# Optimization experiments

Measured on AMD Instinct MI355X. Metric: run time of the kernel, lower is better.

Reference implementation:

```python
import jax, jax.numpy as jnp
import numpy as np

SMOOTH = 1e-5  # MONAI DiceLoss smooth_nr / smooth_dr defaults
BETA = 1.0


def setup_inputs() -> dict:
    key = jax.random.key(0)
    k1, k2, k3 = jax.random.split(key, 3)
    B, C, H, W = 8, 16, 512, 512
    outputs = jax.random.normal(k1, (B, C, H, W), dtype=jnp.float32)
    targets = jax.random.randint(k2, (B, 1, H, W), 0, C, dtype=jnp.int64)
    matrix_penalty = jax.random.uniform(k3, (C, C), dtype=jnp.float32)
    return {
        "outputs": outputs,
        "targets": targets,
        "matrix_penalty": matrix_penalty,
        "N_classes": C,
        "Npixels": H * W,
        "length_targets": B,
        "total_batch": B,
    }


def _domino_loss(outputs, matrix_penalty, t, N_classes, total_batch):
    # outputs: [B, C, H, W] logits; t: [B, H, W] int labels
    logp = jax.nn.log_softmax(outputs, axis=1)          # [B, C, H, W]
    probs = jnp.exp(logp)
    probs_bhwc = jnp.moveaxis(probs, 1, -1)             # [B, H, W, C]
    onehot = jax.nn.one_hot(t, N_classes, dtype=outputs.dtype)  # [B, H, W, C]

    # Cross-entropy term (mean over all pixels), as in CrossEntropyLoss
    ce = -jnp.mean(jnp.sum(onehot * jnp.moveaxis(logp, 1, -1), axis=-1))

    # Dice term (softmax probs vs one-hot target, per batch x class, mean)
    inter = jnp.sum(probs_bhwc * onehot, axis=(1, 2))   # [B, C]
    denom = jnp.sum(probs_bhwc, axis=(1, 2)) + jnp.sum(onehot, axis=(1, 2))
    dice = jnp.mean(1.0 - (2.0 * inter + SMOOTH) / (denom + SMOOTH))

    # DOMINO penalty: per pixel, one_hot(target)^T @ matrix_penalty @ softmax(logits)
    # = matrix_penalty[target] . probs  (gather row instead of tiny matmul)
    pen_rows = matrix_penalty[t]                        # [B, H, W, C]
    penalty = jnp.sum(pen_rows * probs_bhwc)

    return ce + dice + BETA * penalty / total_batch


def reference(outputs, targets, matrix_penalty, N_classes, Npixels, length_targets, total_batch):
    t = targets[:, 0].astype(jnp.int32)                 # [B, H, W]
    return _domino_loss(outputs, matrix_penalty, t, N_classes, total_batch)
```

## Files before the change

### kernel.cpp

```cpp
#include <hip/hip_runtime.h>

#define NC      16
#define HW      (512 * 512)
#define NB      8
#define BPB     128
#define NBLK    (NB * BPB)
#define THREADS 256
#define CHUNK   (HW / BPB)
#define VITERS  (CHUNK / (THREADS * 2))
#define SMOOTH  1e-5f

__global__ __launch_bounds__(THREADS) void domino_main(
    const float* __restrict__ logits,
    const int*   __restrict__ tgt,
    const float* __restrict__ penalty,
    float*       __restrict__ P)
{
    __shared__ float pen_t[NC * NC];
    __shared__ float red[4][34];

    const int tid = threadIdx.x;
    const int b   = blockIdx.x / BPB;
    const int blk = blockIdx.x % BPB;

    if (tid < NC * NC) {
        const int r = tid / NC, c = tid % NC;
        pen_t[c * NC + r] = penalty[tid];
    }
    __syncthreads();

    float inter_acc[NC], denom_acc[NC];
#pragma unroll
    for (int c = 0; c < NC; ++c) { inter_acc[c] = 0.f; denom_acc[c] = 0.f; }
    float ce_acc = 0.f, pen_acc = 0.f;

    const float* ob = logits + (size_t)b * NC * HW;
    const int*   tb = tgt    + (size_t)b * HW;

#pragma unroll
    for (int k = 0; k < VITERS; ++k) {
        const int g   = blk * (CHUNK / 2) + k * THREADS + tid;
        const int pix = g * 2;

        float2 x[NC];
#pragma unroll
        for (int c = 0; c < NC; ++c)
            x[c] = *(const float2*)(ob + (size_t)c * HW + pix);
        const int2 t2 = *(const int2*)(tb + pix);

#define PROC(F, TT) do {                                                    \
        const int t = (TT);                                                 \
        float m = -3.402823466e+38f;                                        \
        _Pragma("unroll")                                                   \
        for (int c = 0; c < NC; ++c) m = fmaxf(m, x[c].F);                  \
        float s = 0.f, xt = 0.f;                                            \
        _Pragma("unroll")                                                   \
        for (int c = 0; c < NC; ++c) {                                      \
            s  += __expf(x[c].F - m);                                       \
            xt += (t == c) ? x[c].F : 0.f;                                  \
        }                                                                   \
        const float inv = 1.0f / s;                                         \
        ce_acc += (__logf(s) + m) - xt;                                     \
        float pdot = 0.f;                                                   \
        _Pragma("unroll")                                                   \
        for (int c = 0; c < NC; ++c) {                                      \
            const float p = __expf(x[c].F - m) * inv;                       \
            denom_acc[c] += p + ((t == c) ? 1.f : 0.f);                     \
            inter_acc[c] += (t == c) ? p : 0.f;                             \
            pdot += pen_t[c * NC + t] * p;                                  \
        }                                                                   \
        pen_acc += pdot;                                                    \
    } while (0)

        PROC(x, t2.x);
        PROC(y, t2.y);
#undef PROC
    }

#pragma unroll
    for (int c = 0; c < NC; ++c) {
#pragma unroll
        for (int off = 32; off; off >>= 1) {
            inter_acc[c] += __shfl_xor(inter_acc[c], off);
            denom_acc[c] += __shfl_xor(denom_acc[c], off);
        }
    }
#pragma unroll
    for (int off = 32; off; off >>= 1) {
        ce_acc  += __shfl_xor(ce_acc,  off);
        pen_acc += __shfl_xor(pen_acc, off);
    }

    const int lane = tid & 63, wid = tid >> 6;
    if (lane == 0) {
#pragma unroll
        for (int c = 0; c < NC; ++c) {
            red[wid][c]      = inter_acc[c];
            red[wid][NC + c] = denom_acc[c];
        }
        red[wid][32] = ce_acc;
        red[wid][33] = pen_acc;
    }
    __syncthreads();

    if (tid < 34) {
        const float v = red[0][tid] + red[1][tid] + red[2][tid] + red[3][tid];
        P[tid * NBLK + blockIdx.x] = v;
    }
}

__global__ __launch_bounds__(128) void domino_final(
    const float* __restrict__ P, float* __restrict__ out)
{
    const int tid = threadIdx.x;
    const int c = tid >> 3, b = tid & 7;

    float inter = 0.f, denom = 0.f;
    const float4* ip = (const float4*)(P + (size_t)c        * NBLK + b * BPB);
    const float4* dp = (const float4*)(P + (size_t)(NC + c) * NBLK + b * BPB);
#pragma unroll 8
    for (int k = 0; k < BPB / 4; ++k) {
        const float4 a = ip[k]; inter += a.x + a.y + a.z + a.w;
        const float4 d = dp[k]; denom += d.x + d.y + d.z + d.w;
    }
    float dice = 1.0f - (2.0f * inter + SMOOTH) / (denom + SMOOTH);

    float ce = 0.f, pen = 0.f;
    const float4* cp = (const float4*)(P + 32 * NBLK + tid * 8);
    const float4* pp = (const float4*)(P + 33 * NBLK + tid * 8);
#pragma unroll
    for (int k = 0; k < 2; ++k) {
        const float4 a = cp[k]; ce  += a.x + a.y + a.z + a.w;
        const float4 d = pp[k]; pen += d.x + d.y + d.z + d.w;
    }

#pragma unroll
    for (int off = 32; off; off >>= 1) {
        dice += __shfl_xor(dice, off);
        ce   += __shfl_xor(ce,   off);
        pen  += __shfl_xor(pen,  off);
    }
    __shared__ float r[3][2];
    const int lane = tid & 63, wid = tid >> 6;
    if (lane == 0) { r[0][wid] = dice; r[1][wid] = ce; r[2][wid] = pen; }
    __syncthreads();
    if (tid == 0) {
        out[0] = (r[1][0] + r[1][1]) * (1.0f / (8.0f * 262144.0f))
               + (r[0][0] + r[0][1]) * (1.0f / 128.0f)
               + (r[2][0] + r[2][1]) * (1.0f / 8.0f);
    }
}

extern "C" void kernel_launch(void* const* d_in, const int* in_sizes, int n_in,
                              void* d_out, int out_size, void* d_ws, size_t ws_size,
                              hipStream_t stream)
{
    const float* logits = (const float*)d_in[0];
    const int*   tgt    = (const int*)d_in[1];
    const float* pen    = (const float*)d_in[2];
    float*       P      = (float*)d_ws;
    float*       out    = (float*)d_out;

    domino_main<<<NBLK, THREADS, 0, stream>>>(logits, tgt, pen, P);
    domino_final<<<1, 128, 0, stream>>>(P, out);
}
```

Measured before the change: 42.17 us.

## Double-buffer logit loads, select target logit via bit tree, widen final reduction

The main kernel's four-iteration loop becomes an explicit software pipeline with two register buffers, so the next chunk's loads are issued before the current chunk is processed. The target logit is now picked with a 4-level binary select tree on the label bits instead of a 16-way compare-accumulate. The final reduction kernel goes from 128 to 1024 threads, with shuffles splitting each bin's sum across lanes. Together these aim to hide memory latency and shorten the serial tail, at the cost of higher register pressure from holding two 16-channel float2 buffers.

Result: slower. 106.4 us (+152.4%).

```diff
diff --git a/kernel.cpp b/kernel.cpp
--- a/kernel.cpp
+++ b/kernel.cpp
@@ -7,7 +7,6 @@
 #define NBLK    (NB * BPB)
 #define THREADS 256
 #define CHUNK   (HW / BPB)
-#define VITERS  (CHUNK / (THREADS * 2))
 #define SMOOTH  1e-5f
 
 __global__ __launch_bounds__(THREADS) void domino_main(
@@ -37,45 +36,59 @@
     const float* ob = logits + (size_t)b * NC * HW;
     const int*   tb = tgt    + (size_t)b * HW;
 
-#pragma unroll
-    for (int k = 0; k < VITERS; ++k) {
-        const int g   = blk * (CHUNK / 2) + k * THREADS + tid;
-        const int pix = g * 2;
-
-        float2 x[NC];
-#pragma unroll
-        for (int c = 0; c < NC; ++c)
-            x[c] = *(const float2*)(ob + (size_t)c * HW + pix);
-        const int2 t2 = *(const int2*)(tb + pix);
-
-#define PROC(F, TT) do {                                                    \
-        const int t = (TT);                                                 \
-        float m = -3.402823466e+38f;                                        \
-        _Pragma("unroll")                                                   \
-        for (int c = 0; c < NC; ++c) m = fmaxf(m, x[c].F);                  \
-        float s = 0.f, xt = 0.f;                                            \
-        _Pragma("unroll")                                                   \
-        for (int c = 0; c < NC; ++c) {                                      \
-            s  += __expf(x[c].F - m);                                       \
-            xt += (t == c) ? x[c].F : 0.f;                                  \
-        }                                                                   \
-        const float inv = 1.0f / s;                                         \
-        ce_acc += (__logf(s) + m) - xt;                                     \
-        float pdot = 0.f;                                                   \
-        _Pragma("unroll")                                                   \
-        for (int c = 0; c < NC; ++c) {                                      \
-            const float p = __expf(x[c].F - m) * inv;                       \
-            denom_acc[c] += p + ((t == c) ? 1.f : 0.f);                     \
-            inter_acc[c] += (t == c) ? p : 0.f;                             \
-            pdot += pen_t[c * NC + t] * p;                                  \
-        }                                                                   \
-        pen_acc += pdot;                                                    \
+#define LOADX(X, T, K) do {                                                  \
+        const int pix = (blk * (CHUNK / 2) + (K) * THREADS + tid) * 2;       \
+        _Pragma("unroll")                                                    \
+        for (int c = 0; c < NC; ++c)                                         \
+            X[c] = *(const float2*)(ob + (size_t)c * HW + pix);              \
+        T = *(const int2*)(tb + pix);                                        \
     } while (0)
 
-        PROC(x, t2.x);
-        PROC(y, t2.y);
+#define PROC(X, F, TT) do {                                                  \
+        const int t = (TT);                                                  \
+        const bool t0 = t & 1, t1 = t & 2, t2 = t & 4, t3 = t & 8;           \
+        float m = -3.402823466e+38f;                                         \
+        _Pragma("unroll")                                                    \
+        for (int c = 0; c < NC; ++c) m = fmaxf(m, X[c].F);                   \
+        float s = 0.f;                                                       \
+        _Pragma("unroll")                                                    \
+        for (int c = 0; c < NC; ++c) s += __expf(X[c].F - m);                \
+        float z[8];                                                          \
+        _Pragma("unroll")                                                    \
+        for (int i = 0; i < 8; ++i) z[i] = t0 ? X[2*i+1].F : X[2*i].F;       \
+        _Pragma("unroll")                                                    \
+        for (int i = 0; i < 4; ++i) z[i] = t1 ? z[2*i+1] : z[2*i];           \
+        z[0] = t2 ? z[2] : z[0];                                             \
+        z[1] = t2 ? z[3] : z[1];                                             \
+        const float xt = t3 ? z[1] : z[0];                                   \
+        const float inv = 1.0f / s;                                          \
+        ce_acc += (__logf(s) + m) - xt;                                      \
+        float pdot = 0.f;                                                    \
+        _Pragma("unroll")                                                    \
+        for (int c = 0; c < NC; ++c) {                                       \
+            const float p = __expf(X[c].F - m) * inv;                        \
+            denom_acc[c] += p + ((t == c) ? 1.f : 0.f);                      \
+            inter_acc[c] += (t == c) ? p : 0.f;                              \
+            pdot += pen_t[c * NC + t] * p;                                   \
+        }                                                                    \
+        pen_acc += pdot;                                                     \
+    } while (0)
+
+#define PROC2(X, T) do { PROC(X, x, T.x); PROC(X, y, T.y); } while (0)
+
+    float2 xA[NC], xB[NC];
+    int2 tA, tB;
+    LOADX(xA, tA, 0);
+    LOADX(xB, tB, 1);
+    PROC2(xA, tA);
+    LOADX(xA, tA, 2);
+    PROC2(xB, tB);
+    LOADX(xB, tB, 3);
+    PROC2(xA, tA);
+    PROC2(xB, tB);
+#undef PROC2
 #undef PROC
-    }
+#undef LOADX
 
 #pragma unroll
     for (int c = 0; c < NC; ++c) {
@@ -109,45 +122,54 @@
     }
 }
 
-__global__ __launch_bounds__(128) void domino_final(
+__global__ __launch_bounds__(1024) void domino_final(
     const float* __restrict__ P, float* __restrict__ out)
 {
+    __shared__ float dice_l[128], ce_l[16], pen_l[16];
+
     const int tid = threadIdx.x;
-    const int c = tid >> 3, b = tid & 7;
+    const int bin = tid >> 3, j = tid & 7;
+    const int c = bin >> 3, b = bin & 7;
 
+    const float4* ip = (const float4*)(P + (size_t)c        * NBLK + b * BPB) + j * 4;
+    const float4* dp = (const float4*)(P + (size_t)(NC + c) * NBLK + b * BPB) + j * 4;
     float inter = 0.f, denom = 0.f;
-    const float4* ip = (const float4*)(P + (size_t)c        * NBLK + b * BPB);
-    const float4* dp = (const float4*)(P + (size_t)(NC + c) * NBLK + b * BPB);
-#pragma unroll 8
-    for (int k = 0; k < BPB / 4; ++k) {
+#pragma unroll
+    for (int k = 0; k < 4; ++k) {
         const float4 a = ip[k]; inter += a.x + a.y + a.z + a.w;
         const float4 d = dp[k]; denom += d.x + d.y + d.z + d.w;
     }
-    float dice = 1.0f - (2.0f * inter + SMOOTH) / (denom + SMOOTH);
+#pragma unroll
+    for (int off = 4; off; off >>= 1) {
+        inter += __shfl_xor(inter, off);
+        denom += __shfl_xor(denom, off);
+    }
+    if (j == 0)
+        dice_l[bin] = 1.0f - (2.0f * inter + SMOOTH) / (denom + SMOOTH);
 
-    float ce = 0.f, pen = 0.f;
-    const float4* cp = (const float4*)(P + 32 * NBLK + tid * 8);
-    const float4* pp = (const float4*)(P + 33 * NBLK + tid * 8);
-#pragma unroll
-    for (int k = 0; k < 2; ++k) {
-        const float4 a = cp[k]; ce  += a.x + a.y + a.z + a.w;
-        const float4 d = pp[k]; pen += d.x + d.y + d.z + d.w;
-    }
-
+    float ce  = P[32 * NBLK + tid];
+    float pen = P[33 * NBLK + tid];
 #pragma unroll
     for (int off = 32; off; off >>= 1) {
-        dice += __shfl_xor(dice, off);
-        ce   += __shfl_xor(ce,   off);
-        pen  += __shfl_xor(pen,  off);
+        ce  += __shfl_xor(ce,  off);
+        pen += __shfl_xor(pen, off);
     }
-    __shared__ float r[3][2];
     const int lane = tid & 63, wid = tid >> 6;
-    if (lane == 0) { r[0][wid] = dice; r[1][wid] = ce; r[2][wid] = pen; }
+    if (lane == 0) { ce_l[wid] = ce; pen_l[wid] = pen; }
     __syncthreads();
-    if (tid == 0) {
-        out[0] = (r[1][0] + r[1][1]) * (1.0f / (8.0f * 262144.0f))
-               + (r[0][0] + r[0][1]) * (1.0f / 128.0f)
-               + (r[2][0] + r[2][1]) * (1.0f / 8.0f);
+
+    if (tid < 64) {
+        float d = dice_l[tid] + dice_l[tid + 64];
+#pragma unroll
+        for (int off = 32; off; off >>= 1) d += __shfl_xor(d, off);
+        if (tid == 0) {
+            float ces = 0.f, pens = 0.f;
+#pragma unroll
+            for (int i = 0; i < 16; ++i) { ces += ce_l[i]; pens += pen_l[i]; }
+            out[0] = ces  * (1.0f / (8.0f * 262144.0f))
+                   + d    * (1.0f / 128.0f)
+                   + pens * (1.0f / 8.0f);
+        }
     }
 }
 
@@ -162,5 +184,5 @@
     float*       out    = (float*)d_out;
 
     domino_main<<<NBLK, THREADS, 0, stream>>>(logits, tgt, pen, P);
-    domino_final<<<1, 128, 0, stream>>>(P, out);
+    domino_final<<<1, 1024, 0, stream>>>(P, out);
 }
```
